# Performance work log

Measured on AMD Instinct MI355X. Metric: run time of the kernel, lower is better.

Reference implementation:

```python
import jax, jax.numpy as jnp
import numpy as np
from jax import lax

K = 3  # ksize (odd)


def _box_mean(x):
    """Edge-clipped k x k mean filter over the last two dims of [B,C,H,W].
    Equivalent to the torch Mean_Filter: sum over the window intersected
    with the image, divided by the actual number of in-bounds pixels."""
    H, W = x.shape[2], x.shape[3]
    sums = lax.reduce_window(x, 0.0, lax.add,
                             window_dimensions=(1, 1, K, K),
                             window_strides=(1, 1, 1, 1),
                             padding='SAME')
    counts = lax.reduce_window(jnp.ones((H, W), x.dtype), 0.0, lax.add,
                               window_dimensions=(K, K),
                               window_strides=(1, 1),
                               padding='SAME')  # [H,W] in-bounds counts
    return sums / counts[None, None, :, :]


def setup_inputs() -> dict:
    key = jax.random.key(0)
    k1, k2, k3 = jax.random.split(key, 3)
    B, C, H, W = 32, 64, 128, 128
    x = jax.random.normal(k1, (B, C, H, W), dtype=jnp.float32)
    # 1x1 conv weight [out_c, in_c] and bias, as in nn.Conv2d(64, 64, 1)
    conv_w = jax.random.normal(k2, (C, C), dtype=jnp.float32) * (1.0 / np.sqrt(C))
    conv_b = jax.random.normal(k3, (C,), dtype=jnp.float32) * 0.01
    return {"x": x, "conv_w": conv_w, "conv_b": conv_b}


def reference(x, conv_w, conv_b):
    # denoising_box forward: x + conv1x1(mean_filter(x))
    x_denoised = _box_mean(x)
    y = jnp.einsum('bchw,oc->bohw', x_denoised, conv_w) + conv_b[None, :, None, None]
    return x + y
```

## Files before the change

kernel.cpp:

```cpp
#include <hip/hip_runtime.h>

#define B_   32
#define C_   64
#define H_   128
#define W_   128
#define HW_  (H_ * W_)
#define CHW_ (C_ * HW_)
#define TH_  4
#define CW_  64

__global__ __launch_bounds__(256, 4) void denoise_fused(
    const float* __restrict__ x, const float* __restrict__ cw,
    const float* __restrict__ cb, float* __restrict__ out)
{
    __shared__ __align__(16) float xd[C_ * CW_];
    __shared__ __align__(16) float Wt[C_ * C_];
    __shared__ float bnd[C_];

    const int t    = threadIdx.x;
    const int b    = blockIdx.x >> 5;
    const int h0   = (blockIdx.x & 31) * TH_;
    const int lane = t & 63;
    const int wid  = t >> 6;
    const int jj   = lane & 15;
    const int sub  = lane >> 4;
    const int m    = wid * 4 + sub;

    for (int i = t; i < C_ * C_; i += 256) {
        int o = i >> 6, c = i & 63;
        xd[o * 64 + ((c + o) & 63)] = cw[i];
    }
    __syncthreads();
    for (int k = t; k < C_ * C_; k += 256) {
        int c = k >> 6, r = k & 63;
        int o = (r >> 2) + ((r & 3) << 4);
        Wt[k] = xd[o * 64 + ((c + o) & 63)];
    }
    __syncthreads();

    const float* xb = x   + (size_t)b * CHW_;
    float*       ob = out + (size_t)b * CHW_;

    float bias[4];
    #pragma unroll
    for (int oi = 0; oi < 4; ++oi) bias[oi] = cb[m + 16 * oi];

    for (int r = 0; r < TH_; ++r) {
        const int h = h0 + r;
        const bool hm = (h > 0), hp = (h < H_ - 1);
        const float rv = 1.f + (hm ? 1.f : 0.f) + (hp ? 1.f : 0.f);
        const float i3 = 1.f / (rv * 3.f);
        const float i2 = 1.f / (rv * 2.f);

        #pragma unroll
        for (int q = 0; q < 2; ++q) {
            float s[4][4];

            #pragma unroll
            for (int p = 0; p < 4; ++p) {
                const int c = 16 * p + m;
                const float* rc = xb + c * HW_ + h * W_ + q * CW_;
                float4 cen = ((const float4*)rc)[jj];
                s[p][0] = cen.x; s[p][1] = cen.y; s[p][2] = cen.z; s[p][3] = cen.w;
                float4 v = cen;
                if (hm) { float4 a = ((const float4*)(rc - W_))[jj]; v.x += a.x; v.y += a.y; v.z += a.z; v.w += a.w; }
                if (hp) { float4 a = ((const float4*)(rc + W_))[jj]; v.x += a.x; v.y += a.y; v.z += a.z; v.w += a.w; }
                float L = __shfl_up(v.w, 1);
                float R = __shfl_down(v.x, 1);
                if (q == 0) {
                    if (jj == 15) {
                        bnd[c] = v.w;
                        const float* rb = rc + CW_;
                        float vr = rb[0];
                        if (hm) vr += rb[-W_];
                        if (hp) vr += rb[W_];
                        R = vr;
                    }
                } else {
                    if (jj == 0) L = bnd[c];
                }
                float4 d;
                d.x = (q == 0 && jj == 0)  ? (v.x + v.y) * i2 : (L + v.x + v.y) * i3;
                d.y = (v.x + v.y + v.z) * i3;
                d.z = (v.y + v.z + v.w) * i3;
                d.w = (q == 1 && jj == 15) ? (v.z + v.w) * i2 : (v.z + v.w + R) * i3;
                ((float4*)xd)[c * 16 + jj] = d;
            }
            __syncthreads();

            float acc[4][4];
            #pragma unroll
            for (int oi = 0; oi < 4; ++oi) {
                acc[oi][0] = s[oi][0] + bias[oi];
                acc[oi][1] = s[oi][1] + bias[oi];
                acc[oi][2] = s[oi][2] + bias[oi];
                acc[oi][3] = s[oi][3] + bias[oi];
            }

            #pragma unroll 4
            for (int c = 0; c < C_; ++c) {
                float4 xv = ((const float4*)xd)[c * 16 + jj];
                float4 wv = *(const float4*)&Wt[c * 64 + m * 4];
                float w4[4] = { wv.x, wv.y, wv.z, wv.w };
                #pragma unroll
                for (int oi = 0; oi < 4; ++oi) {
                    acc[oi][0] += w4[oi] * xv.x;
                    acc[oi][1] += w4[oi] * xv.y;
                    acc[oi][2] += w4[oi] * xv.z;
                    acc[oi][3] += w4[oi] * xv.w;
                }
            }

            #pragma unroll
            for (int oi = 0; oi < 4; ++oi) {
                float4 res;
                res.x = acc[oi][0]; res.y = acc[oi][1];
                res.z = acc[oi][2]; res.w = acc[oi][3];
                ((float4*)(ob + (m + 16 * oi) * HW_ + h * W_ + q * CW_))[jj] = res;
            }
            __syncthreads();
        }
    }
}

extern "C" void kernel_launch(void* const* d_in, const int* in_sizes, int n_in,
                              void* d_out, int out_size, void* d_ws, size_t ws_size,
                              hipStream_t stream) {
    const float* x  = (const float*)d_in[0];
    const float* cw = (const float*)d_in[1];
    const float* cb = (const float*)d_in[2];
    float* out = (float*)d_out;
    dim3 grid(B_ * (H_ / TH_));
    dim3 block(256);
    hipLaunchKernelGGL(denoise_fused, grid, block, 0, stream, x, cw, cb, out);
}
```

Before: 305.2 us.

## Use fp16 MFMA for 1x1 conv with per-wave row ownership

Replaces the scalar FP32 channel-mixing loop with MFMA 16x16x32 f16 instructions. Weights are held in registers as half8 fragments, and the box-filtered tile goes to a per-wave XOR-swizzled LDS buffer in fp16. Each wave now owns one image row, so the block-wide __syncthreads barriers and the shared bnd boundary exchange are gone. The grid order is also remapped to interleave work across blocks. This cuts ALU time on a memory-heavy kernel, but fp16 rounding of activations and weights adds error, and each block re-reads the residual x from global memory.

```diff
diff --git a/kernel.cpp b/kernel.cpp
--- a/kernel.cpp
+++ b/kernel.cpp
@@ -6,119 +6,145 @@
 #define W_   128
 #define HW_  (H_ * W_)
 #define CHW_ (C_ * HW_)
-#define TH_  4
-#define CW_  64
+
+typedef _Float16 half8 __attribute__((ext_vector_type(8)));
+typedef float f32x4 __attribute__((ext_vector_type(4)));
+
+static __device__ inline ushort f2h(float f) {
+    union { _Float16 h; ushort u; } cv;
+    cv.h = (_Float16)f;
+    return cv.u;
+}
 
 __global__ __launch_bounds__(256, 4) void denoise_fused(
     const float* __restrict__ x, const float* __restrict__ cw,
     const float* __restrict__ cb, float* __restrict__ out)
 {
-    __shared__ __align__(16) float xd[C_ * CW_];
-    __shared__ __align__(16) float Wt[C_ * C_];
-    __shared__ float bnd[C_];
+    __shared__ ushort Abuf[4][64 * 64];
 
     const int t    = threadIdx.x;
-    const int b    = blockIdx.x >> 5;
-    const int h0   = (blockIdx.x & 31) * TH_;
     const int lane = t & 63;
     const int wid  = t >> 6;
-    const int jj   = lane & 15;
-    const int sub  = lane >> 4;
-    const int m    = wid * 4 + sub;
+    const int r    = lane & 15;
+    const int g    = lane >> 4;
 
-    for (int i = t; i < C_ * C_; i += 256) {
-        int o = i >> 6, c = i & 63;
-        xd[o * 64 + ((c + o) & 63)] = cw[i];
-    }
-    __syncthreads();
-    for (int k = t; k < C_ * C_; k += 256) {
-        int c = k >> 6, r = k & 63;
-        int o = (r >> 2) + ((r & 3) << 4);
-        Wt[k] = xd[o * 64 + ((c + o) & 63)];
-    }
-    __syncthreads();
+    const int work   = (blockIdx.x & 7) * 128 + (blockIdx.x >> 3);
+    const int row_id = work * 4 + wid;
+    const int b = row_id >> 7;
+    const int h = row_id & 127;
 
     const float* xb = x   + (size_t)b * CHW_;
     float*       ob = out + (size_t)b * CHW_;
 
-    float bias[4];
+    half8 Wf[2][4];
     #pragma unroll
-    for (int oi = 0; oi < 4; ++oi) bias[oi] = cb[m + 16 * oi];
+    for (int k = 0; k < 2; ++k)
+        #pragma unroll
+        for (int n = 0; n < 4; ++n) {
+            const float* wp = cw + (n * 16 + r) * 64 + k * 32 + g * 8;
+            float4 w0 = *(const float4*)wp;
+            float4 w1 = *(const float4*)(wp + 4);
+            half8 hh;
+            hh[0] = (_Float16)w0.x; hh[1] = (_Float16)w0.y;
+            hh[2] = (_Float16)w0.z; hh[3] = (_Float16)w0.w;
+            hh[4] = (_Float16)w1.x; hh[5] = (_Float16)w1.y;
+            hh[6] = (_Float16)w1.z; hh[7] = (_Float16)w1.w;
+            Wf[k][n] = hh;
+        }
 
-    for (int r = 0; r < TH_; ++r) {
-        const int h = h0 + r;
-        const bool hm = (h > 0), hp = (h < H_ - 1);
-        const float rv = 1.f + (hm ? 1.f : 0.f) + (hp ? 1.f : 0.f);
-        const float i3 = 1.f / (rv * 3.f);
-        const float i2 = 1.f / (rv * 2.f);
+    float bias4[4];
+    #pragma unroll
+    for (int n = 0; n < 4; ++n) bias4[n] = cb[n * 16 + r];
+
+    const bool hm = (h > 0), hp = (h < H_ - 1);
+    const float rv = 1.f + (hm ? 1.f : 0.f) + (hp ? 1.f : 0.f);
+    const float i3 = 1.f / (rv * 3.f);
+    const float i2 = 1.f / (rv * 2.f);
+
+    ushort* A = Abuf[wid];
+
+    #pragma unroll
+    for (int q = 0; q < 2; ++q) {
+        #pragma unroll
+        for (int p = 0; p < 16; ++p) {
+            const int c = g * 16 + p;
+            const float* rc = xb + c * HW_ + h * W_ + q * 64;
+            float4 v = ((const float4*)rc)[r];
+            if (hm) { float4 a = ((const float4*)(rc - W_))[r]; v.x += a.x; v.y += a.y; v.z += a.z; v.w += a.w; }
+            if (hp) { float4 a = ((const float4*)(rc + W_))[r]; v.x += a.x; v.y += a.y; v.z += a.z; v.w += a.w; }
+            float L = __shfl_up(v.w, 1);
+            float R = __shfl_down(v.x, 1);
+            if (q == 0 && r == 15) {
+                const float* rb = rc + 64;
+                float vr = rb[0];
+                if (hm) vr += rb[-W_];
+                if (hp) vr += rb[W_];
+                R = vr;
+            }
+            if (q == 1 && r == 0) {
+                const float* lb = rc - 1;
+                float vl = lb[0];
+                if (hm) vl += lb[-W_];
+                if (hp) vl += lb[W_];
+                L = vl;
+            }
+            float d4[4];
+            d4[0] = (q == 0 && r == 0)  ? (v.x + v.y) * i2 : (L + v.x + v.y) * i3;
+            d4[1] = (v.x + v.y + v.z) * i3;
+            d4[2] = (v.y + v.z + v.w) * i3;
+            d4[3] = (q == 1 && r == 15) ? (v.z + v.w) * i2 : (v.z + v.w + R) * i3;
+            #pragma unroll
+            for (int e = 0; e < 4; ++e) {
+                const int px = 4 * r + e;
+                const int pp = (px ^ (px >> 3)) & 7;
+                A[px * 64 + (c ^ (pp << 3))] = f2h(d4[e]);
+            }
+        }
+
+        f32x4 acc[4][4];
+        #pragma unroll
+        for (int n = 0; n < 4; ++n) {
+            const int o = n * 16 + r;
+            #pragma unroll
+            for (int m = 0; m < 4; ++m) {
+                const float* rp = xb + o * HW_ + h * W_ + q * 64 + m * 16 + 4 * g;
+                float4 xr = *(const float4*)rp;
+                f32x4 a;
+                a[0] = xr.x + bias4[n]; a[1] = xr.y + bias4[n];
+                a[2] = xr.z + bias4[n]; a[3] = xr.w + bias4[n];
+                acc[m][n] = a;
+            }
+        }
 
         #pragma unroll
-        for (int q = 0; q < 2; ++q) {
-            float s[4][4];
+        for (int k = 0; k < 2; ++k) {
+            half8 Af[4];
+            #pragma unroll
+            for (int m = 0; m < 4; ++m) {
+                const int px = m * 16 + r;
+                const int pp = (px ^ (px >> 3)) & 7;
+                const int slot = (4 * k + g) ^ pp;
+                Af[m] = *(const half8*)&A[px * 64 + slot * 8];
+            }
+            #pragma unroll
+            for (int n = 0; n < 4; ++n)
+                #pragma unroll
+                for (int m = 0; m < 4; ++m)
+                    acc[m][n] = __builtin_amdgcn_mfma_f32_16x16x32_f16(
+                        Af[m], Wf[k][n], acc[m][n], 0, 0, 0);
+        }
 
+        #pragma unroll
+        for (int n = 0; n < 4; ++n) {
+            const int o = n * 16 + r;
             #pragma unroll
-            for (int p = 0; p < 4; ++p) {
-                const int c = 16 * p + m;
-                const float* rc = xb + c * HW_ + h * W_ + q * CW_;
-                float4 cen = ((const float4*)rc)[jj];
-                s[p][0] = cen.x; s[p][1] = cen.y; s[p][2] = cen.z; s[p][3] = cen.w;
-                float4 v = cen;
-                if (hm) { float4 a = ((const float4*)(rc - W_))[jj]; v.x += a.x; v.y += a.y; v.z += a.z; v.w += a.w; }
-                if (hp) { float4 a = ((const float4*)(rc + W_))[jj]; v.x += a.x; v.y += a.y; v.z += a.z; v.w += a.w; }
-                float L = __shfl_up(v.w, 1);
-                float R = __shfl_down(v.x, 1);
-                if (q == 0) {
-                    if (jj == 15) {
-                        bnd[c] = v.w;
-                        const float* rb = rc + CW_;
-                        float vr = rb[0];
-                        if (hm) vr += rb[-W_];
-                        if (hp) vr += rb[W_];
-                        R = vr;
-                    }
-                } else {
-                    if (jj == 0) L = bnd[c];
-                }
-                float4 d;
-                d.x = (q == 0 && jj == 0)  ? (v.x + v.y) * i2 : (L + v.x + v.y) * i3;
-                d.y = (v.x + v.y + v.z) * i3;
-                d.z = (v.y + v.z + v.w) * i3;
-                d.w = (q == 1 && jj == 15) ? (v.z + v.w) * i2 : (v.z + v.w + R) * i3;
-                ((float4*)xd)[c * 16 + jj] = d;
+            for (int m = 0; m < 4; ++m) {
+                float* op = ob + o * HW_ + h * W_ + q * 64 + m * 16 + 4 * g;
+                float4 res;
+                res.x = acc[m][n][0]; res.y = acc[m][n][1];
+                res.z = acc[m][n][2]; res.w = acc[m][n][3];
+                *(float4*)op = res;
             }
-            __syncthreads();
-
-            float acc[4][4];
-            #pragma unroll
-            for (int oi = 0; oi < 4; ++oi) {
-                acc[oi][0] = s[oi][0] + bias[oi];
-                acc[oi][1] = s[oi][1] + bias[oi];
-                acc[oi][2] = s[oi][2] + bias[oi];
-                acc[oi][3] = s[oi][3] + bias[oi];
-            }
-
-            #pragma unroll 4
-            for (int c = 0; c < C_; ++c) {
-                float4 xv = ((const float4*)xd)[c * 16 + jj];
-                float4 wv = *(const float4*)&Wt[c * 64 + m * 4];
-                float w4[4] = { wv.x, wv.y, wv.z, wv.w };
-                #pragma unroll
-                for (int oi = 0; oi < 4; ++oi) {
-                    acc[oi][0] += w4[oi] * xv.x;
-                    acc[oi][1] += w4[oi] * xv.y;
-                    acc[oi][2] += w4[oi] * xv.z;
-                    acc[oi][3] += w4[oi] * xv.w;
-                }
-            }
-
-            #pragma unroll
-            for (int oi = 0; oi < 4; ++oi) {
-                float4 res;
-                res.x = acc[oi][0]; res.y = acc[oi][1];
-                res.z = acc[oi][2]; res.w = acc[oi][3];
-                ((float4*)(ob + (m + 16 * oi) * HW_ + h * W_ + q * CW_))[jj] = res;
-            }
-            __syncthreads();
         }
     }
 }
@@ -130,7 +156,7 @@
     const float* cw = (const float*)d_in[1];
     const float* cb = (const float*)d_in[2];
     float* out = (float*)d_out;
-    dim3 grid(B_ * (H_ / TH_));
+    dim3 grid(1024);
     dim3 block(256);
     hipLaunchKernelGGL(denoise_fused, grid, block, 0, stream, x, cw, cb, out);
 }
```

New measurement: 478.6 us. 56.8% more time.
